# Performance work log

Measured on AMD Instinct MI355X. Metric: run time of the kernel, lower is better.

## Reference

```python
import math
import jax, jax.numpy as jnp
import numpy as np

B, L0, IN, D, H, FF, PRED = 16, 4096, 8, 256, 8, 1024, 24
NLAYERS = 3
FACTOR = 5

def _u(L):
    return max(1, min(FACTOR * math.ceil(math.log(L + 1)), L))

def _ln(x, g, b, eps=1e-5):
    m = x.mean(-1, keepdims=True)
    v = ((x - m) ** 2).mean(-1, keepdims=True)
    return (x - m) * jax.lax.rsqrt(v + eps) * g + b

def _prob_attn(h, idx, wq, bq, wk, bk, wv, bv, wo, bo):
    B_, L, Dm = h.shape
    dk = Dm // H
    scale = 1.0 / math.sqrt(dk)
    def proj(w, b):
        return (h @ w + b).reshape(B_, L, H, dk).transpose(0, 2, 1, 3)
    Q, K, V = proj(wq, bq), proj(wk, bk), proj(wv, bv)  # [B,H,L,dk]
    u = idx.shape[0]
    Ks = K[:, :, idx, :]                                   # sampled keys [B,H,u,dk]
    scores = jnp.einsum('bhld,bhud->bhlu', Q, Ks) * scale
    M = scores.max(-1) - scores.mean(-1)                   # sparsity score [B,H,L]
    top = jax.lax.top_k(M, u)[1]                           # top-u queries [B,H,u]
    Qt = jnp.take_along_axis(Q, top[..., None], axis=2)    # [B,H,u,dk]
    attn = jax.nn.softmax(jnp.einsum('bhud,bhld->bhul', Qt, K) * scale, axis=-1)
    ctx_top = jnp.einsum('bhul,bhld->bhud', attn, V)       # [B,H,u,dk]
    ctx = jnp.broadcast_to(V.mean(2, keepdims=True), (B_, H, L, dk))
    bh = B_ * H
    ctx = ctx.reshape(bh, L, dk).at[jnp.arange(bh)[:, None], top.reshape(bh, u)].set(ctx_top.reshape(bh, u, dk))
    ctx = ctx.reshape(B_, H, L, dk).transpose(0, 2, 1, 3).reshape(B_, L, Dm)
    return ctx @ wo + bo

def _distill(x, w, b):
    # Conv1d(k=3,pad=1) + ELU + MaxPool1d(2)
    xc = x.transpose(0, 2, 1)  # [B,D,L]
    y = jax.lax.conv_general_dilated(xc, w, (1,), [(1, 1)], dimension_numbers=('NCH', 'OIH', 'NCH')) + b[None, :, None]
    y = jax.nn.elu(y)
    y = jax.lax.reduce_window(y, -jnp.inf, jax.lax.max, (1, 1, 2), (1, 1, 2), 'VALID')
    return y.transpose(0, 2, 1)

def _forward(x, in_w, in_b, pos_emb, qw, qb, kw, kb, vw, vb, ow, ob, f1w, f1b, f2w, f2b, n1g, n1b, n2g, n2b, cw, cb, fcw, fcb, idxs):
    Bx, L, _ = x.shape
    h = x @ in_w + in_b + pos_emb[None, :L]
    for i in range(NLAYERS):
        a = _prob_attn(h, idxs[i], qw[i], qb[i], kw[i], kb[i], vw[i], vb[i], ow[i], ob[i])
        h = _ln(h + a, n1g[i], n1b[i])
        f = jax.nn.gelu(h @ f1w[i] + f1b[i], approximate=False) @ f2w[i] + f2b[i]
        h = _ln(h + f, n2g[i], n2b[i])
        if i < NLAYERS - 1:
            h = _distill(h, cw[i], cb[i])
    return h[:, -1, :] @ fcw + fcb

def setup_inputs():
    key = jax.random.key(0)
    ks = jax.random.split(key, 16)
    s = 0.02
    d = {}
    d['x'] = jax.random.normal(ks[0], (B, L0, IN), jnp.float32)
    Ls = [L0, L0 // 2, L0 // 4]
    for i, Li in enumerate(Ls):
        d[f'idx{i}'] = jax.random.randint(ks[1 + i], (_u(Li),), 0, Li, jnp.int32)
    d['in_w'] = jax.random.normal(ks[4], (IN, D)) * s
    d['in_b'] = jnp.zeros((D,))
    d['pos_emb'] = jax.random.normal(ks[5], (L0, D)) * s
    d['qw'] = jax.random.normal(ks[6], (NLAYERS, D, D)) * s
    d['qb'] = jnp.zeros((NLAYERS, D))
    d['kw'] = jax.random.normal(ks[7], (NLAYERS, D, D)) * s
    d['kb'] = jnp.zeros((NLAYERS, D))
    d['vw'] = jax.random.normal(ks[8], (NLAYERS, D, D)) * s
    d['vb'] = jnp.zeros((NLAYERS, D))
    d['ow'] = jax.random.normal(ks[9], (NLAYERS, D, D)) * s
    d['ob'] = jnp.zeros((NLAYERS, D))
    d['f1w'] = jax.random.normal(ks[10], (NLAYERS, D, FF)) * s
    d['f1b'] = jnp.zeros((NLAYERS, FF))
    d['f2w'] = jax.random.normal(ks[11], (NLAYERS, FF, D)) * s
    d['f2b'] = jnp.zeros((NLAYERS, D))
    d['n1g'] = jnp.ones((NLAYERS, D))
    d['n1b'] = jnp.zeros((NLAYERS, D))
    d['n2g'] = jnp.ones((NLAYERS, D))
    d['n2b'] = jnp.zeros((NLAYERS, D))
    d['cw'] = jax.random.normal(ks[12], (NLAYERS - 1, D, D, 3)) * s
    d['cb'] = jnp.zeros((NLAYERS - 1, D))
    d['fcw'] = jax.random.normal(ks[13], (D, PRED)) * s
    d['fcb'] = jnp.zeros((PRED,))
    return d

def reference(x, idx0, idx1, idx2, in_w, in_b, pos_emb, qw, qb, kw, kb, vw, vb, ow, ob, f1w, f1b, f2w, f2b, n1g, n1b, n2g, n2b, cw, cb, fcw, fcb):
    return _forward(x, in_w, in_b, pos_emb, qw, qb, kw, kb, vw, vb, ow, ob, f1w, f1b, f2w, f2b, n1g, n1b, n2g, n2b, cw, cb, fcw, fcb, (idx0, idx1, idx2))
```

## Files before the change

kernel.cpp:

```cpp
#include <hip/hip_runtime.h>
#include <hip/hip_bf16.h>
#include <math.h>

typedef __hip_bfloat16 bf16;
typedef __attribute__((ext_vector_type(8))) short short8;
typedef __attribute__((ext_vector_type(4))) float floatx4;

#define B_    16
#define L0_   4096
#define IN_   8
#define D_    256
#define H_    8
#define DK_   32
#define FF_   1024
#define PRED_ 24
#define UMAX_ 48
#define NS_   4
#define NSV_  8
#define SCALE_ 0.17677669529663687f

__device__ __forceinline__ float b2f(bf16 v) { return __bfloat162float(v); }
__device__ __forceinline__ bf16  f2b(float v){ return __float2bfloat16(v); }
__device__ __forceinline__ float gelu_exact(float x){
  return 0.5f * x * (1.0f + erff(x * 0.7071067811865476f));
}
__device__ __forceinline__ float eluf(float x){ return x > 0.f ? x : (expf(x) - 1.f); }
__device__ __forceinline__ float ldf(const void* p, size_t i, int f){
  return f ? ((const float*)p)[i] : b2f(((const bf16*)p)[i]);
}
__device__ __forceinline__ void gld16(const void* g, const short* l){
  __builtin_amdgcn_global_load_lds(
      (const __attribute__((address_space(1))) unsigned int*)g,
      (__attribute__((address_space(3))) unsigned int*)l, 16, 0, 0);
}
__device__ __forceinline__ void unpack8(uint4 v, float* o){
  o[0] = __uint_as_float(v.x << 16); o[1] = __uint_as_float(v.x & 0xffff0000u);
  o[2] = __uint_as_float(v.y << 16); o[3] = __uint_as_float(v.y & 0xffff0000u);
  o[4] = __uint_as_float(v.z << 16); o[5] = __uint_as_float(v.z & 0xffff0000u);
  o[6] = __uint_as_float(v.w << 16); o[7] = __uint_as_float(v.w & 0xffff0000u);
}
__device__ __forceinline__ void ld_row32(const bf16* p, float* o){
  const uint4* q = (const uint4*)p;
  uint4 a = q[0], b = q[1], c = q[2], d = q[3];
  unpack8(a, o); unpack8(b, o + 8); unpack8(c, o + 16); unpack8(d, o + 24);
}

__global__ __launch_bounds__(256) void detect_mode_kernel(
    const unsigned short* __restrict__ x16, int* __restrict__ flag,
    bf16* __restrict__ zbuf)
{
  int tid = threadIdx.x;
  if (tid < 32) zbuf[tid] = f2b(0.f);
  int cnt = 0;
  for (int i = tid; i < 512; i += 256) {
    unsigned short v = x16[2 * i];
    int expo = (v >> 7) & 0xFF;
    if (expo >= 0x90) cnt++;
  }
  __shared__ int red[256];
  red[tid] = cnt;
  __syncthreads();
  for (int s = 128; s > 0; s >>= 1) {
    if (tid < s) red[tid] += red[tid + s];
    __syncthreads();
  }
  if (tid == 0) flag[0] = (red[0] > 8) ? 1 : 0;
}

__global__ __launch_bounds__(256) void canon_kernel(
    const void* __restrict__ src, bf16* __restrict__ dst, int n,
    const int* __restrict__ flag)
{
  int i = blockIdx.x * 256 + threadIdx.x;
  if (i >= n) return;
  dst[i] = f2b(ldf(src, i, flag[0]));
}

__global__ __launch_bounds__(256) void transpose_w_kernel(
    const void* __restrict__ src, bf16* __restrict__ dst, int K, int N,
    const int* __restrict__ flag)
{
  int i = blockIdx.x * 256 + threadIdx.x;
  if (i >= K * N) return;
  size_t off = (size_t)blockIdx.y * K * N;
  int k = i / N, n = i % N;
  dst[off + (size_t)n * K + k] = f2b(ldf(src, off + i, flag[0]));
}

__global__ __launch_bounds__(256) void transpose_cw_kernel(
    const void* __restrict__ src, bf16* __restrict__ dst,
    const int* __restrict__ flag)
{
  int i = blockIdx.x * 256 + threadIdx.x;
  if (i >= D_ * D_ * 3) return;
  size_t off = (size_t)blockIdx.y * D_ * D_ * 3;
  int o = i / (D_ * 3), c = (i / 3) % D_, t = i % 3;
  dst[off + ((size_t)t * D_ + o) * D_ + c] = f2b(ldf(src, off + i, flag[0]));
}

__global__ __launch_bounds__(256) void embed_kernel(
    const void* __restrict__ x, const void* __restrict__ in_w,
    const void* __restrict__ in_b, const void* __restrict__ pos,
    const int* __restrict__ flag, bf16* __restrict__ h)
{
  int token = blockIdx.x;
  int d = threadIdx.x;
  int l = token % L0_;
  int f = flag[0];
  float s = ldf(in_b, d, f) + ldf(pos, (size_t)l * D_ + d, f);
#pragma unroll
  for (int k = 0; k < IN_; ++k)
    s += ldf(x, (size_t)token * IN_ + k, f) * ldf(in_w, k * D_ + d, f);
  h[(size_t)token * D_ + d] = f2b(s);
}

template<int ACT, int HM>
__global__ __launch_bounds__(256) void mfma_gemm(
    const bf16* __restrict__ A, const bf16* __restrict__ Wt,
    const bf16* __restrict__ bias, bf16* __restrict__ C,
    int M, int N, int K, int Lsh)
{
  __shared__ short As[128 * 32];
  __shared__ short Bs[128 * 32];
  int tid = threadIdx.x;
  int w = tid >> 6, lane = tid & 63;
  int ln = lane & 15, qd = lane >> 4;
  int bm = blockIdx.y << 7, bn = blockIdx.x << 7;
  int wm = (w >> 1) << 6, wn = (w & 1) << 6;

  floatx4 acc[4][4];
#pragma unroll
  for (int mi = 0; mi < 4; ++mi)
#pragma unroll
    for (int ni = 0; ni < 4; ++ni) {
      acc[mi][ni][0] = 0.f; acc[mi][ni][1] = 0.f;
      acc[mi][ni][2] = 0.f; acc[mi][ni][3] = 0.f;
    }

  int s0 = (w << 7) + lane, s1 = s0 + 64;
  int r0 = s0 >> 2, c0 = (s0 & 3) ^ (r0 & 3);
  int r1 = s1 >> 2, c1 = (s1 & 3) ^ (r1 & 3);
  const bf16* pA0 = A + (size_t)(bm + r0) * K + (c0 << 3);
  const bf16* pA1 = A + (size_t)(bm + r1) * K + (c1 << 3);
  const bf16* pB0 = Wt + (size_t)(bn + r0) * K + (c0 << 3);
  const bf16* pB1 = Wt + (size_t)(bn + r1) * K + (c1 << 3);
  short* ldsA = As + (w << 10);
  short* ldsB = Bs + (w << 10);

  for (int k0 = 0; k0 < K; k0 += 32) {
    __syncthreads();
    gld16(pA0 + k0, ldsA);
    gld16(pA1 + k0, ldsA + 512);
    gld16(pB0 + k0, ldsB);
    gld16(pB1 + k0, ldsB + 512);
    __syncthreads();
    short8 af[4], bff[4];
#pragma unroll
    for (int mi = 0; mi < 4; ++mi) {
      int r = wm + mi * 16 + ln;
      af[mi] = *(const short8*)(As + (r << 5) + ((qd ^ (r & 3)) << 3));
    }
#pragma unroll
    for (int ni = 0; ni < 4; ++ni) {
      int r = wn + ni * 16 + ln;
      bff[ni] = *(const short8*)(Bs + (r << 5) + ((qd ^ (r & 3)) << 3));
    }
#pragma unroll
    for (int mi = 0; mi < 4; ++mi)
#pragma unroll
      for (int ni = 0; ni < 4; ++ni)
        acc[mi][ni] = __builtin_amdgcn_mfma_f32_16x16x32_bf16(
            af[mi], bff[ni], acc[mi][ni], 0, 0, 0);
  }

#pragma unroll
  for (int ni = 0; ni < 4; ++ni) {
    int col = bn + wn + ni * 16 + ln;
    float bv = b2f(bias[col]);
    int hh = col >> 5, dk = col & 31;
#pragma unroll
    for (int mi = 0; mi < 4; ++mi) {
      int row = bm + wm + mi * 16 + (qd << 2);
#pragma unroll
      for (int r = 0; r < 4; ++r) {
        float v = acc[mi][ni][r] + bv;
        if (ACT == 1) v = gelu_exact(v);
        if (HM) {
          int rr = row + r;
          int bb = rr >> Lsh, ll = rr & ((1 << Lsh) - 1);
          C[((((size_t)(bb * H_ + hh)) << Lsh) + ll) * 32 + dk] = f2b(v);
        } else {
          C[(size_t)(row + r) * N + col] = f2b(v);
        }
      }
    }
  }
}

__global__ __launch_bounds__(256) void mfma_conv_distill(
    const bf16* __restrict__ hsrc, const bf16* __restrict__ WtC,
    const bf16* __restrict__ cb, bf16* __restrict__ outp,
    const bf16* __restrict__ zbuf, int L)
{
  __shared__ short As[128 * 32];
  __shared__ short Bs[128 * 32];
  int tid = threadIdx.x;
  int w = tid >> 6, lane = tid & 63;
  int ln = lane & 15, qd = lane >> 4;
  int bn = blockIdx.x << 7;
  int bpb = L >> 7;
  int b = blockIdx.y / bpb;
  int p0 = (blockIdx.y % bpb) << 7;
  int wm = (w >> 1) << 6, wn = (w & 1) << 6;

  floatx4 acc[4][4];
#pragma unroll
  for (int mi = 0; mi < 4; ++mi)
#pragma unroll
    for (int ni = 0; ni < 4; ++ni) {
      acc[mi][ni][0] = 0.f; acc[mi][ni][1] = 0.f;
      acc[mi][ni][2] = 0.f; acc[mi][ni][3] = 0.f;
    }

  int s0 = (w << 7) + lane, s1 = s0 + 64;
  int r0 = s0 >> 2, c0 = (s0 & 3) ^ (r0 & 3);
  int r1 = s1 >> 2, c1 = (s1 & 3) ^ (r1 & 3);
  short* ldsA = As + (w << 10);
  short* ldsB = Bs + (w << 10);

  for (int tap = 0; tap < 3; ++tap) {
    const bf16* wt = WtC + (size_t)tap * D_ * D_;
    int pos0 = p0 + r0 + tap - 1;
    int pos1 = p0 + r1 + tap - 1;
    const bf16* gA0 = (pos0 >= 0 && pos0 < L)
        ? hsrc + ((size_t)b * L + pos0) * D_ + (c0 << 3) : zbuf;
    const bf16* gA1 = (pos1 >= 0 && pos1 < L)
        ? hsrc + ((size_t)b * L + pos1) * D_ + (c1 << 3) : zbuf;
    int stepA0 = (pos0 >= 0 && pos0 < L) ? 1 : 0;
    int stepA1 = (pos1 >= 0 && pos1 < L) ? 1 : 0;
    const bf16* gB0 = wt + (size_t)(bn + r0) * D_ + (c0 << 3);
    const bf16* gB1 = wt + (size_t)(bn + r1) * D_ + (c1 << 3);
    for (int k0 = 0; k0 < D_; k0 += 32) {
      __syncthreads();
      gld16(gA0 + (size_t)k0 * stepA0, ldsA);
      gld16(gA1 + (size_t)k0 * stepA1, ldsA + 512);
      gld16(gB0 + k0, ldsB);
      gld16(gB1 + k0, ldsB + 512);
      __syncthreads();
      short8 af[4], bff[4];
#pragma unroll
      for (int mi = 0; mi < 4; ++mi) {
        int r = wm + mi * 16 + ln;
        af[mi] = *(const short8*)(As + (r << 5) + ((qd ^ (r & 3)) << 3));
      }
#pragma unroll
      for (int ni = 0; ni < 4; ++ni) {
        int r = wn + ni * 16 + ln;
        bff[ni] = *(const short8*)(Bs + (r << 5) + ((qd ^ (r & 3)) << 3));
      }
#pragma unroll
      for (int mi = 0; mi < 4; ++mi)
#pragma unroll
        for (int ni = 0; ni < 4; ++ni)
          acc[mi][ni] = __builtin_amdgcn_mfma_f32_16x16x32_bf16(
              af[mi], bff[ni], acc[mi][ni], 0, 0, 0);
    }
  }

  int Lh = L >> 1;
#pragma unroll
  for (int ni = 0; ni < 4; ++ni) {
    int col = bn + wn + ni * 16 + ln;
    float bv = b2f(cb[col]);
#pragma unroll
    for (int mi = 0; mi < 4; ++mi) {
      float y0 = eluf(acc[mi][ni][0] + bv);
      float y1 = eluf(acc[mi][ni][1] + bv);
      float y2 = eluf(acc[mi][ni][2] + bv);
      float y3 = eluf(acc[mi][ni][3] + bv);
      int prow = (p0 + wm + mi * 16 + (qd << 2)) >> 1;
      outp[((size_t)b * Lh + prow) * D_ + col]     = f2b(fmaxf(y0, y1));
      outp[((size_t)b * Lh + prow + 1) * D_ + col] = f2b(fmaxf(y2, y3));
    }
  }
}

__global__ __launch_bounds__(256) void prob_scores_kernel(
    const bf16* __restrict__ Qh, const bf16* __restrict__ Kh,
    const int* __restrict__ idx, float* __restrict__ Mout, int L, int u)
{
  __shared__ float ks[UMAX_][32];
  int tid = threadIdx.x;
  int bpb = L >> 8;
  int bh = blockIdx.x / bpb;
  int l  = (blockIdx.x % bpb) * 256 + tid;
  if (tid < u * 4) {
    int t = tid >> 2, c = tid & 3;
    int ls = idx[t];
    if (ls < 0) ls = 0; if (ls >= L) ls = L - 1;
    uint4 v = *(const uint4*)(Kh + ((size_t)bh * L + ls) * 32 + c * 8);
    unpack8(v, &ks[t][c * 8]);
  }
  __syncthreads();
  float qv[32];
  ld_row32(Qh + ((size_t)bh * L + l) * 32, qv);
  float mx = -3.4e38f, sm = 0.f;
  for (int t = 0; t < u; ++t) {
    float s = 0.f;
#pragma unroll
    for (int j4 = 0; j4 < 8; ++j4) {
      float4 k4 = *(const float4*)&ks[t][j4 * 4];
      s += qv[4*j4+0]*k4.x + qv[4*j4+1]*k4.y + qv[4*j4+2]*k4.z + qv[4*j4+3]*k4.w;
    }
    s *= SCALE_;
    mx = fmaxf(mx, s);
    sm += s;
  }
  Mout[(size_t)bh * L + l] = mx - sm / (float)u;
}

__global__ __launch_bounds__(256) void topk_kernel(
    const float* __restrict__ M, int* __restrict__ top, int L, int u)
{
  __shared__ unsigned int hist[256];
  __shared__ unsigned int prefS, kS;
  __shared__ int cntG, tieCnt;
  __shared__ int tieList[256];
  int bh = blockIdx.x;
  int tid = threadIdx.x;
  int w = tid >> 6, lane = tid & 63;
  int nper = L >> 8;

  unsigned int key[16];
  for (int i = 0; i < nper; ++i) {
    unsigned int ub = __float_as_uint(M[(size_t)bh * L + i * 256 + tid]);
    key[i] = (ub & 0x80000000u) ? ~ub : (ub | 0x80000000u);
  }

  unsigned int pref = 0, k = (unsigned int)u;
  for (int round = 0; round < 4; ++round) {
    int shift = 24 - (round << 3);
    hist[tid] = 0;
    __syncthreads();
    for (int i = 0; i < nper; ++i) {
      unsigned int kk = key[i];
      if (round == 0 || (kk >> (shift + 8)) == pref)
        atomicAdd(&hist[(kk >> shift) & 0xFFu], 1u);
    }
    __syncthreads();
    if (w == 0) {
      int d0 = lane << 2;
      unsigned int h0 = hist[d0], h1 = hist[d0 + 1];
      unsigned int h2 = hist[d0 + 2], h3 = hist[d0 + 3];
      unsigned int lsum = h0 + h1 + h2 + h3;
      unsigned int incl = lsum;
#pragma unroll
      for (int off = 1; off < 64; off <<= 1) {
        unsigned int o = __shfl_down(incl, off);
        if (lane + off < 64) incl += o;
      }
      unsigned int e3 = incl - lsum;
      unsigned int e2 = e3 + h3;
      unsigned int e1 = e2 + h2;
      unsigned int e0 = e1 + h1;
      if (e3 < k && k <= e3 + h3) { prefS = (pref << 8) | (d0 + 3); kS = k - e3; }
      if (e2 < k && k <= e2 + h2) { prefS = (pref << 8) | (d0 + 2); kS = k - e2; }
      if (e1 < k && k <= e1 + h1) { prefS = (pref << 8) | (d0 + 1); kS = k - e1; }
      if (e0 < k && k <= e0 + h0) { prefS = (pref << 8) | (d0 + 0); kS = k - e0; }
    }
    __syncthreads();
    pref = prefS;
    k = kS;
    __syncthreads();
  }

  unsigned int T = pref;
  if (tid == 0) { cntG = 0; tieCnt = 0; }
  __syncthreads();
  for (int i = 0; i < nper; ++i) {
    unsigned int kk = key[i];
    int lidx = i * 256 + tid;
    if (kk > T) {
      int pos = atomicAdd(&cntG, 1);
      if (pos < u) top[bh * u + pos] = lidx;
    } else if (kk == T) {
      int tpos = atomicAdd(&tieCnt, 1);
      if (tpos < 256) tieList[tpos] = lidx;
    }
  }
  __syncthreads();
  if (tid == 0) {
    int base = cntG;
    int E = tieCnt; if (E > 256) E = 256;
    for (int t = 0; t < (int)k && base + t < u; ++t) {
      int best = 0x7fffffff, bj = -1;
      for (int j = 0; j < E; ++j) {
        int v = tieList[j];
        if (v >= 0 && v < best) { best = v; bj = j; }
      }
      if (bj >= 0) { tieList[bj] = -1; top[bh * u + base + t] = best; }
      else top[bh * u + base + t] = 0;
    }
  }
}

__global__ __launch_bounds__(256) void topq_attn_mfma(
    const bf16* __restrict__ Qh, const bf16* __restrict__ Kh,
    const bf16* __restrict__ Vh, const int* __restrict__ top,
    float* __restrict__ part_m, float* __restrict__ part_s,
    float* __restrict__ part_acc, int L, int u)
{
  __shared__ short Qs[64 * 32];
  __shared__ short Ks[128 * 32];
  __shared__ short Vs[128 * 32];
  __shared__ short Ps[4][64 * 32];
  __shared__ float mrow[64];
  __shared__ float redm[4][64];
  __shared__ float redl[4][64];

  int bh = blockIdx.x, sl = blockIdx.y;
  int tid = threadIdx.x;
  int w = tid >> 6, lane = tid & 63;
  int ln = lane & 15, qd = lane >> 4;
  int Ls = L / NS_;
  int lbase = sl * Ls;
  const bf16* Kbase = Kh + (size_t)bh * L * 32;
  const bf16* Vbase = Vh + (size_t)bh * L * 32;

  {
    int r = tid >> 2, cpos = tid & 3, corig = cpos ^ (r & 3);
    uint4 v = make_uint4(0, 0, 0, 0);
    if (r < u) {
      int lq = top[bh * u + r];
      if (lq < 0) lq = 0; if (lq >= L) lq = L - 1;
      v = *(const uint4*)(Qh + ((size_t)bh * L + lq) * 32 + corig * 8);
    }
    *(uint4*)(Qs + r * 32 + cpos * 8) = v;
  }
  __syncthreads();

  short8 aq[4];
#pragma unroll
  for (int mi = 0; mi < 4; ++mi) {
    int r = mi * 16 + ln;
    aq[mi] = *(const short8*)(Qs + (r << 5) + ((qd ^ (r & 3)) << 3));
  }

  int s0 = (w << 7) + lane, s1 = s0 + 64;
  int r0 = s0 >> 2, c0 = (s0 & 3) ^ (r0 & 3);
  int r1 = s1 >> 2, c1 = (s1 & 3) ^ (r1 & 3);
  short* ldsK = Ks + (w << 10);
  short* ldsV = Vs + (w << 10);
  int nch = Ls >> 7;

  float m_run[16];
#pragma unroll
  for (int i = 0; i < 16; ++i) m_run[i] = -3.4e38f;

  for (int ch = 0; ch < nch; ++ch) {
    int tok0 = lbase + (ch << 7);
    __syncthreads();
    gld16(Kbase + (size_t)(tok0 + r0) * 32 + (c0 << 3), ldsK);
    gld16(Kbase + (size_t)(tok0 + r1) * 32 + (c1 << 3), ldsK + 512);
    __syncthreads();
    short8 bk[2];
#pragma unroll
    for (int ni = 0; ni < 2; ++ni) {
      int r = (w << 5) + ni * 16 + ln;
      bk[ni] = *(const short8*)(Ks + (r << 5) + ((qd ^ (r & 3)) << 3));
    }
#pragma unroll
    for (int mi = 0; mi < 4; ++mi)
#pragma unroll
      for (int ni = 0; ni < 2; ++ni) {
        floatx4 s = {0.f, 0.f, 0.f, 0.f};
        s = __builtin_amdgcn_mfma_f32_16x16x32_bf16(aq[mi], bk[ni], s, 0, 0, 0);
#pragma unroll
        for (int r = 0; r < 4; ++r)
          m_run[mi * 4 + r] = fmaxf(m_run[mi * 4 + r], s[r] * SCALE_);
      }
  }
#pragma unroll
  for (int i = 0; i < 16; ++i) {
    float v = m_run[i];
    v = fmaxf(v, __shfl_xor(v, 1));
    v = fmaxf(v, __shfl_xor(v, 2));
    v = fmaxf(v, __shfl_xor(v, 4));
    v = fmaxf(v, __shfl_xor(v, 8));
    m_run[i] = v;
  }
  if (ln == 0) {
#pragma unroll
    for (int mi = 0; mi < 4; ++mi)
#pragma unroll
      for (int r = 0; r < 4; ++r)
        redm[w][mi * 16 + qd * 4 + r] = m_run[mi * 4 + r];
  }
  __syncthreads();
  if (tid < 64)
    mrow[tid] = fmaxf(fmaxf(redm[0][tid], redm[1][tid]),
                      fmaxf(redm[2][tid], redm[3][tid]));
  __syncthreads();

  float l_run[16];
#pragma unroll
  for (int i = 0; i < 16; ++i) l_run[i] = 0.f;
  floatx4 oacc[4][2];
#pragma unroll
  for (int mi = 0; mi < 4; ++mi)
#pragma unroll
    for (int ni = 0; ni < 2; ++ni) {
      oacc[mi][ni][0] = 0.f; oacc[mi][ni][1] = 0.f;
      oacc[mi][ni][2] = 0.f; oacc[mi][ni][3] = 0.f;
    }
  bf16* myPs = (bf16*)Ps[w];

  for (int ch = 0; ch < nch; ++ch) {
    int tok0 = lbase + (ch << 7);
    __syncthreads();
    gld16(Kbase + (size_t)(tok0 + r0) * 32 + (c0 << 3), ldsK);
    gld16(Kbase + (size_t)(tok0 + r1) * 32 + (c1 << 3), ldsK + 512);
    gld16(Vbase + (size_t)(tok0 + r0) * 32 + (c0 << 3), ldsV);
    gld16(Vbase + (size_t)(tok0 + r1) * 32 + (c1 << 3), ldsV + 512);
    __syncthreads();
    short8 bk[2];
#pragma unroll
    for (int ni = 0; ni < 2; ++ni) {
      int r = (w << 5) + ni * 16 + ln;
      bk[ni] = *(const short8*)(Ks + (r << 5) + ((qd ^ (r & 3)) << 3));
    }
#pragma unroll
    for (int mi = 0; mi < 4; ++mi)
#pragma unroll
      for (int ni = 0; ni < 2; ++ni) {
        floatx4 s = {0.f, 0.f, 0.f, 0.f};
        s = __builtin_amdgcn_mfma_f32_16x16x32_bf16(aq[mi], bk[ni], s, 0, 0, 0);
#pragma unroll
        for (int r = 0; r < 4; ++r) {
          int row = mi * 16 + qd * 4 + r;
          float p = expf(s[r] * SCALE_ - mrow[row]);
          l_run[mi * 4 + r] += p;
          int tl = ni * 16 + ln;
          myPs[(row << 5) + (((tl >> 3) ^ (row & 3)) << 3) + (tl & 7)] = f2b(p);
        }
      }
    __syncthreads();
    short8 ap[4];
#pragma unroll
    for (int mi = 0; mi < 4; ++mi) {
      int r = mi * 16 + ln;
      ap[mi] = *(const short8*)((short*)myPs + (r << 5) + ((qd ^ (r & 3)) << 3));
    }
    short8 bv[2];
#pragma unroll
    for (int ni = 0; ni < 2; ++ni) {
      short tmp[8];
#pragma unroll
      for (int j = 0; j < 8; ++j) {
        int tok = (w << 5) + (qd << 3) + j;
        int dk = ni * 16 + ln;
        tmp[j] = Vs[(tok << 5) + (((dk >> 3) ^ (tok & 3)) << 3) + (dk & 7)];
      }
      bv[ni] = *(short8*)tmp;
    }
#pragma unroll
    for (int mi = 0; mi < 4; ++mi)
#pragma unroll
      for (int ni = 0; ni < 2; ++ni)
        oacc[mi][ni] = __builtin_amdgcn_mfma_f32_16x16x32_bf16(
            ap[mi], bv[ni], oacc[mi][ni], 0, 0, 0);
  }

#pragma unroll
  for (int i = 0; i < 16; ++i) {
    float v = l_run[i];
    v += __shfl_xor(v, 1); v += __shfl_xor(v, 2);
    v += __shfl_xor(v, 4); v += __shfl_xor(v, 8);
    l_run[i] = v;
  }
  if (ln == 0) {
#pragma unroll
    for (int mi = 0; mi < 4; ++mi)
#pragma unroll
      for (int r = 0; r < 4; ++r)
        redl[w][mi * 16 + qd * 4 + r] = l_run[mi * 4 + r];
  }
  __syncthreads();

  size_t pb = (size_t)sl * (B_ * H_) + bh;
  if (tid < UMAX_) {
    part_m[pb * UMAX_ + tid] = mrow[tid];
    part_s[pb * UMAX_ + tid] =
        redl[0][tid] + redl[1][tid] + redl[2][tid] + redl[3][tid];
  }
#pragma unroll
  for (int mi = 0; mi < 4; ++mi) {
#pragma unroll
    for (int ni = 0; ni < 2; ++ni) {
#pragma unroll
      for (int r = 0; r < 4; ++r) {
        int row = mi * 16 + qd * 4 + r;
        if (row < UMAX_) {
          int dk = ni * 16 + ln;
          part_acc[((pb * UMAX_ + row) << 7) + (w << 5) + dk] = oacc[mi][ni][r];
        }
      }
    }
  }
}

__global__ __launch_bounds__(256) void attn_combine_kernel(
    const float* __restrict__ part_m, const float* __restrict__ part_s,
    const float* __restrict__ part_acc, float* __restrict__ ctx_top, int u)
{
  int bh = blockIdx.x;
  for (int i = threadIdx.x; i < u * 32; i += 256) {
    int q = i >> 5, dk = i & 31;
    float M = -3.4e38f;
#pragma unroll
    for (int s = 0; s < NS_; ++s)
      M = fmaxf(M, part_m[((size_t)s * (B_ * H_) + bh) * UMAX_ + q]);
    float num = 0.f, den = 0.f;
#pragma unroll
    for (int s = 0; s < NS_; ++s) {
      size_t pb = (size_t)s * (B_ * H_) + bh;
      float e = expf(part_m[pb * UMAX_ + q] - M);
      float a = 0.f;
#pragma unroll
      for (int w = 0; w < 4; ++w)
        a += part_acc[((pb * UMAX_ + q) << 7) + (w << 5) + dk];
      num += a * e;
      den += part_s[pb * UMAX_ + q] * e;
    }
    ctx_top[((size_t)bh * u + q) * 32 + dk] = num / den;
  }
}

__global__ __launch_bounds__(256) void vmean_part_kernel(
    const bf16* __restrict__ Vh, float* __restrict__ vpart, int L)
{
  int blk = blockIdx.x;
  int bh = blk / NSV_, s = blk % NSV_;
  int tid = threadIdx.x;
  int dk = tid & 31, lg = tid >> 5;
  int Ls = L / NSV_;
  int l0 = s * Ls;
  float acc = 0.f;
  for (int l = lg; l < Ls; l += 8)
    acc += b2f(Vh[((size_t)bh * L + l0 + l) * 32 + dk]);
  __shared__ float red[256];
  red[tid] = acc;
  __syncthreads();
  for (int st = 128; st >= 32; st >>= 1) {
    if (tid < st) red[tid] += red[tid + st];
    __syncthreads();
  }
  if (tid < 32) vpart[(size_t)blk * 32 + tid] = red[tid];
}

__global__ __launch_bounds__(32) void vmean_comb_kernel(
    const float* __restrict__ vpart, float* __restrict__ vmean, int L)
{
  int bh = blockIdx.x;
  int dk = threadIdx.x;
  float s = 0.f;
#pragma unroll
  for (int i = 0; i < NSV_; ++i)
    s += vpart[((size_t)bh * NSV_ + i) * 32 + dk];
  vmean[bh * 32 + dk] = s / (float)L;
}

__global__ __launch_bounds__(256) void fill_ctx_kernel(
    const float* __restrict__ vmean, bf16* __restrict__ ctx, int L)
{
  size_t i = (size_t)blockIdx.x * 256 + threadIdx.x;
  int d = (int)(i % D_);
  size_t token = i / D_;
  int b = (int)(token / L);
  ctx[i] = f2b(vmean[(b * H_ + d / DK_) * DK_ + (d & (DK_ - 1))]);
}

__global__ __launch_bounds__(256) void scatter_kernel(
    const float* __restrict__ ctx_top, const int* __restrict__ top,
    bf16* __restrict__ ctx, int L, int u)
{
  int t = blockIdx.x * 256 + threadIdx.x;
  int total = B_ * H_ * u * DK_;
  if (t >= total) return;
  int j  = t % DK_;
  int uu = (t / DK_) % u;
  int hh = (t / (DK_ * u)) % H_;
  int b  = t / (DK_ * u * H_);
  int lq = top[(b * H_ + hh) * u + uu];
  if (lq < 0) lq = 0; if (lq >= L) lq = L - 1;
  ctx[((size_t)b * L + lq) * D_ + hh * DK_ + j] =
      f2b(ctx_top[(size_t)((b * H_ + hh) * u + uu) * DK_ + j]);
}

__global__ __launch_bounds__(256) void add_ln_kernel(
    bf16* __restrict__ h, const bf16* __restrict__ r,
    const bf16* __restrict__ g, const bf16* __restrict__ be)
{
  size_t t = blockIdx.x;
  int d = threadIdx.x;
  __shared__ float lds4[4];
  float v = b2f(h[t * D_ + d]) + b2f(r[t * D_ + d]);
  float s = v;
  for (int off = 32; off; off >>= 1) s += __shfl_down(s, off);
  if ((threadIdx.x & 63) == 0) lds4[threadIdx.x >> 6] = s;
  __syncthreads();
  float mean = (lds4[0] + lds4[1] + lds4[2] + lds4[3]) * (1.f / D_);
  __syncthreads();
  float dv = v - mean;
  float q = dv * dv;
  for (int off = 32; off; off >>= 1) q += __shfl_down(q, off);
  if ((threadIdx.x & 63) == 0) lds4[threadIdx.x >> 6] = q;
  __syncthreads();
  float var = (lds4[0] + lds4[1] + lds4[2] + lds4[3]) * (1.f / D_);
  h[t * D_ + d] = f2b(dv * rsqrtf(var + 1e-5f) * b2f(g[d]) + b2f(be[d]));
}

__global__ __launch_bounds__(256) void copy_bf16_kernel(
    bf16* __restrict__ dst, const bf16* __restrict__ src, size_t n)
{
  size_t i = (size_t)blockIdx.x * 256 + threadIdx.x;
  if (i < n) dst[i] = src[i];
}

__global__ __launch_bounds__(64) void final_fc_kernel(
    const bf16* __restrict__ h, const bf16* __restrict__ fcw,
    const bf16* __restrict__ fcb, void* __restrict__ out, int L,
    const int* __restrict__ flag)
{
  int b = blockIdx.x;
  int p = threadIdx.x;
  if (p >= PRED_) return;
  const bf16* hr = h + ((size_t)b * L + (L - 1)) * D_;
  float s = b2f(fcb[p]);
  for (int d = 0; d < D_; ++d) s += b2f(hr[d]) * b2f(fcw[d * PRED_ + p]);
  if (flag[0]) ((float*)out)[b * PRED_ + p] = s;
  else         ((bf16*)out)[b * PRED_ + p]  = f2b(s);
}

extern "C" void kernel_launch(void* const* d_in, const int* in_sizes, int n_in,
                              void* d_out, int out_size, void* d_ws, size_t ws_size,
                              hipStream_t stream)
{
  const size_t hsz = (size_t)B_ * L0_ * D_;
  char* wsc = (char*)d_ws;
  bf16* h  = (bf16*)wsc;
  bf16* Qh = (bf16*)(wsc + hsz * 2);
  bf16* Kh = (bf16*)(wsc + hsz * 4);
  bf16* Vh = (bf16*)(wsc + hsz * 6);
  char* misc = wsc + hsz * 8;
  float* Mbuf    = (float*)misc;
  float* ctx_top = Mbuf + (size_t)B_ * H_ * L0_;
  float* vmean   = ctx_top + (size_t)B_ * H_ * UMAX_ * DK_;
  int*   topbuf  = (int*)(vmean + B_ * H_ * DK_);
  int*   flag    = topbuf + B_ * H_ * UMAX_;
  float* part_m  = (float*)(flag + 4);
  float* part_s  = part_m + (size_t)NS_ * B_ * H_ * UMAX_;
  float* part_acc= part_s + (size_t)NS_ * B_ * H_ * UMAX_;
  float* vpart   = part_acc + (size_t)NS_ * B_ * H_ * UMAX_ * 128;
  bf16*  zbuf    = (bf16*)(vpart + (size_t)B_ * H_ * NSV_ * 32);
  bf16*  canon   = zbuf + 32;

  bf16* qwT  = canon;
  bf16* kwT  = qwT  + 3 * 65536;
  bf16* vwT  = kwT  + 3 * 65536;
  bf16* owT  = vwT  + 3 * 65536;
  bf16* f1wT = owT  + 3 * 65536;
  bf16* f2wT = f1wT + 3 * 262144;
  bf16* cwT  = f2wT + 3 * 262144;
  bf16* smallc = cwT + 2 * 196608;

  bf16* ctxb = Vh;
  bf16* ab   = Qh;
  bf16* t1   = Kh;
  bf16* hnext = Kh;

  detect_mode_kernel<<<1, 256, 0, stream>>>((const unsigned short*)d_in[0], flag, zbuf);

  const int cidx[13] = {8, 10, 12, 14, 16, 18, 19, 20, 21, 22, 24, 25, 26};
  bf16* cptr[27] = {};
  {
    bf16* p = smallc;
    for (int t = 0; t < 13; ++t) {
      int i = cidx[t];
      int n = in_sizes[i];
      cptr[i] = p;
      canon_kernel<<<(n + 255) / 256, 256, 0, stream>>>(d_in[i], p, n, flag);
      p += (n + 7) & ~7;
    }
  }
  transpose_w_kernel<<<dim3(256, 3), 256, 0, stream>>>(d_in[7],  qwT,  256, 256, flag);
  transpose_w_kernel<<<dim3(256, 3), 256, 0, stream>>>(d_in[9],  kwT,  256, 256, flag);
  transpose_w_kernel<<<dim3(256, 3), 256, 0, stream>>>(d_in[11], vwT,  256, 256, flag);
  transpose_w_kernel<<<dim3(256, 3), 256, 0, stream>>>(d_in[13], owT,  256, 256, flag);
  transpose_w_kernel<<<dim3(1024, 3), 256, 0, stream>>>(d_in[15], f1wT, 256, 1024, flag);
  transpose_w_kernel<<<dim3(1024, 3), 256, 0, stream>>>(d_in[17], f2wT, 1024, 256, flag);
  transpose_cw_kernel<<<dim3(768, 2), 256, 0, stream>>>(d_in[23], cwT, flag);

  const int* idx[3] = {(const int*)d_in[1], (const int*)d_in[2], (const int*)d_in[3]};
  int us[3] = {in_sizes[1], in_sizes[2], in_sizes[3]};

  embed_kernel<<<B_ * L0_, 256, 0, stream>>>(d_in[0], d_in[4], d_in[5], d_in[6], flag, h);

  int L = L0_;
  for (int i = 0; i < 3; ++i) {
    int tokens = B_ * L;
    int u = us[i];
    int Lsh = 31 - __builtin_clz(L);
    dim3 gDD(2, tokens / 128);
    mfma_gemm<0,1><<<gDD, 256, 0, stream>>>(h, qwT + (size_t)i * 65536, cptr[8]  + i * D_, Qh, tokens, D_, D_, Lsh);
    mfma_gemm<0,1><<<gDD, 256, 0, stream>>>(h, kwT + (size_t)i * 65536, cptr[10] + i * D_, Kh, tokens, D_, D_, Lsh);
    mfma_gemm<0,1><<<gDD, 256, 0, stream>>>(h, vwT + (size_t)i * 65536, cptr[12] + i * D_, Vh, tokens, D_, D_, Lsh);

    prob_scores_kernel<<<B_ * H_ * (L / 256), 256, 0, stream>>>(Qh, Kh, idx[i], Mbuf, L, u);
    topk_kernel<<<B_ * H_, 256, 0, stream>>>(Mbuf, topbuf, L, u);
    topq_attn_mfma<<<dim3(B_ * H_, NS_), 256, 0, stream>>>(
        Qh, Kh, Vh, topbuf, part_m, part_s, part_acc, L, u);
    attn_combine_kernel<<<B_ * H_, 256, 0, stream>>>(part_m, part_s, part_acc, ctx_top, u);
    vmean_part_kernel<<<B_ * H_ * NSV_, 256, 0, stream>>>(Vh, vpart, L);
    vmean_comb_kernel<<<B_ * H_, 32, 0, stream>>>(vpart, vmean, L);
    fill_ctx_kernel<<<(unsigned)(((size_t)tokens * D_) / 256), 256, 0, stream>>>(vmean, ctxb, L);
    scatter_kernel<<<(B_ * H_ * u * DK_ + 255) / 256, 256, 0, stream>>>(ctx_top, topbuf, ctxb, L, u);
    mfma_gemm<0,0><<<gDD, 256, 0, stream>>>(ctxb, owT + (size_t)i * 65536, cptr[14] + i * D_, ab, tokens, D_, D_, 0);

    add_ln_kernel<<<tokens, 256, 0, stream>>>(h, ab, cptr[19] + i * D_, cptr[20] + i * D_);

    const int CH = 16384;
    for (int c0 = 0; c0 < tokens; c0 += CH) {
      int cm = (tokens - c0 < CH) ? (tokens - c0) : CH;
      mfma_gemm<1,0><<<dim3(8, cm / 128), 256, 0, stream>>>(
          h + (size_t)c0 * D_, f1wT + (size_t)i * 262144, cptr[16] + i * FF_, t1, cm, FF_, D_, 0);
      mfma_gemm<0,0><<<dim3(2, cm / 128), 256, 0, stream>>>(
          t1, f2wT + (size_t)i * 262144, cptr[18] + i * D_, ab + (size_t)c0 * D_, cm, D_, FF_, 0);
    }
    add_ln_kernel<<<tokens, 256, 0, stream>>>(h, ab, cptr[21] + i * D_, cptr[22] + i * D_);

    if (i < 2) {
      int Lh = L / 2;
      mfma_conv_distill<<<dim3(2, B_ * (L / 128)), 256, 0, stream>>>(
          h, cwT + (size_t)i * 196608, cptr[24] + i * D_, hnext, zbuf, L);
      size_t n = (size_t)B_ * Lh * D_;
      copy_bf16_kernel<<<(unsigned)((n + 255) / 256), 256, 0, stream>>>(h, hnext, n);
      L = Lh;
    }
  }
  final_fc_kernel<<<B_, 64, 0, stream>>>(h, cptr[25], cptr[26], d_out, L, flag);
}
```

Measured before the change: 1.432 ms.

## Fuse QKV GEMMs, deepen GEMM K-tile, vectorize LayerNorm, embed and fill kernels

The three Q/K/V projections become one GEMM over a concatenated 768-wide weight, with per-part bias and head-major output to Q/K/V buffers separated by a stride. This removes two launches and two extra reads of h. The shared GEMM kernel now stages a 64-wide K slice per barrier pair with an 8-way XOR swizzle, which halves the number of syncs but doubles LDS use per block. add_ln becomes one wave per row with vectorized loads and xor-shuffle reductions, and the embed and fill_ctx kernels each process 8 tokens per block.

```diff
diff --git a/kernel.cpp b/kernel.cpp
--- a/kernel.cpp
+++ b/kernel.cpp
@@ -39,6 +39,14 @@
   o[4] = __uint_as_float(v.z << 16); o[5] = __uint_as_float(v.z & 0xffff0000u);
   o[6] = __uint_as_float(v.w << 16); o[7] = __uint_as_float(v.w & 0xffff0000u);
 }
+__device__ __forceinline__ void unpack4(uint2 v, float* o){
+  o[0] = __uint_as_float(v.x << 16); o[1] = __uint_as_float(v.x & 0xffff0000u);
+  o[2] = __uint_as_float(v.y << 16); o[3] = __uint_as_float(v.y & 0xffff0000u);
+}
+__device__ __forceinline__ unsigned pack2(float a, float b){
+  bf16 x = f2b(a), y = f2b(b);
+  return (unsigned)*(unsigned short*)&x | ((unsigned)*(unsigned short*)&y << 16);
+}
 __device__ __forceinline__ void ld_row32(const bf16* p, float* o){
   const uint4* q = (const uint4*)p;
   uint4 a = q[0], b = q[1], c = q[2], d = q[3];
@@ -78,13 +86,13 @@
 
 __global__ __launch_bounds__(256) void transpose_w_kernel(
     const void* __restrict__ src, bf16* __restrict__ dst, int K, int N,
-    const int* __restrict__ flag)
+    const int* __restrict__ flag, int lstride)
 {
   int i = blockIdx.x * 256 + threadIdx.x;
   if (i >= K * N) return;
-  size_t off = (size_t)blockIdx.y * K * N;
+  size_t soff = (size_t)blockIdx.y * K * N;
   int k = i / N, n = i % N;
-  dst[off + (size_t)n * K + k] = f2b(ldf(src, off + i, flag[0]));
+  dst[(size_t)blockIdx.y * lstride + (size_t)n * K + k] = f2b(ldf(src, soff + i, flag[0]));
 }
 
 __global__ __launch_bounds__(256) void transpose_cw_kernel(
@@ -103,25 +111,34 @@
     const void* __restrict__ in_b, const void* __restrict__ pos,
     const int* __restrict__ flag, bf16* __restrict__ h)
 {
-  int token = blockIdx.x;
   int d = threadIdx.x;
-  int l = token % L0_;
   int f = flag[0];
-  float s = ldf(in_b, d, f) + ldf(pos, (size_t)l * D_ + d, f);
-#pragma unroll
-  for (int k = 0; k < IN_; ++k)
-    s += ldf(x, (size_t)token * IN_ + k, f) * ldf(in_w, k * D_ + d, f);
-  h[(size_t)token * D_ + d] = f2b(s);
+  float wcol[IN_];
+#pragma unroll
+  for (int k = 0; k < IN_; ++k) wcol[k] = ldf(in_w, k * D_ + d, f);
+  float bd = ldf(in_b, d, f);
+  int t0 = blockIdx.x * 8;
+#pragma unroll
+  for (int t = 0; t < 8; ++t) {
+    int token = t0 + t;
+    int l = token & (L0_ - 1);
+    float s = bd + ldf(pos, (size_t)l * D_ + d, f);
+#pragma unroll
+    for (int k = 0; k < IN_; ++k)
+      s += ldf(x, (size_t)token * IN_ + k, f) * wcol[k];
+    h[(size_t)token * D_ + d] = f2b(s);
+  }
 }
 
 template<int ACT, int HM>
 __global__ __launch_bounds__(256) void mfma_gemm(
     const bf16* __restrict__ A, const bf16* __restrict__ Wt,
-    const bf16* __restrict__ bias, bf16* __restrict__ C,
-    int M, int N, int K, int Lsh)
-{
-  __shared__ short As[128 * 32];
-  __shared__ short Bs[128 * 32];
+    const bf16* __restrict__ b0, const bf16* __restrict__ b1,
+    const bf16* __restrict__ b2, bf16* __restrict__ C,
+    int M, int N, int K, int Lsh, size_t partStride)
+{
+  __shared__ short As[128 * 64];
+  __shared__ short Bs[128 * 64];
   int tid = threadIdx.x;
   int w = tid >> 6, lane = tid & 63;
   int ln = lane & 15, qd = lane >> 4;
@@ -137,47 +154,64 @@
       acc[mi][ni][2] = 0.f; acc[mi][ni][3] = 0.f;
     }
 
-  int s0 = (w << 7) + lane, s1 = s0 + 64;
-  int r0 = s0 >> 2, c0 = (s0 & 3) ^ (r0 & 3);
-  int r1 = s1 >> 2, c1 = (s1 & 3) ^ (r1 & 3);
-  const bf16* pA0 = A + (size_t)(bm + r0) * K + (c0 << 3);
-  const bf16* pA1 = A + (size_t)(bm + r1) * K + (c1 << 3);
-  const bf16* pB0 = Wt + (size_t)(bn + r0) * K + (c0 << 3);
-  const bf16* pB1 = Wt + (size_t)(bn + r1) * K + (c1 << 3);
-  short* ldsA = As + (w << 10);
-  short* ldsB = Bs + (w << 10);
-
-  for (int k0 = 0; k0 < K; k0 += 32) {
-    __syncthreads();
-    gld16(pA0 + k0, ldsA);
-    gld16(pA1 + k0, ldsA + 512);
-    gld16(pB0 + k0, ldsB);
-    gld16(pB1 + k0, ldsB + 512);
-    __syncthreads();
-    short8 af[4], bff[4];
-#pragma unroll
-    for (int mi = 0; mi < 4; ++mi) {
-      int r = wm + mi * 16 + ln;
-      af[mi] = *(const short8*)(As + (r << 5) + ((qd ^ (r & 3)) << 3));
-    }
-#pragma unroll
-    for (int ni = 0; ni < 4; ++ni) {
-      int r = wn + ni * 16 + ln;
-      bff[ni] = *(const short8*)(Bs + (r << 5) + ((qd ^ (r & 3)) << 3));
-    }
-#pragma unroll
-    for (int mi = 0; mi < 4; ++mi)
-#pragma unroll
-      for (int ni = 0; ni < 4; ++ni)
-        acc[mi][ni] = __builtin_amdgcn_mfma_f32_16x16x32_bf16(
-            af[mi], bff[ni], acc[mi][ni], 0, 0, 0);
+  int rr[4], ofs[4];
+#pragma unroll
+  for (int t = 0; t < 4; ++t) {
+    int p = (w << 8) + (t << 6) + lane;
+    int r = p >> 3;
+    ofs[t] = (((p & 7) ^ (r & 7)) << 3);
+    rr[t] = r;
+  }
+  const bf16* pA[4]; const bf16* pB[4]; short* dst[4];
+#pragma unroll
+  for (int t = 0; t < 4; ++t) {
+    pA[t] = A + (size_t)(bm + rr[t]) * K + ofs[t];
+    pB[t] = Wt + (size_t)(bn + rr[t]) * K + ofs[t];
+    dst[t] = (short*)(As) + (((w << 2) + t) << 9);
+  }
+
+  for (int k0 = 0; k0 < K; k0 += 64) {
+    __syncthreads();
+#pragma unroll
+    for (int t = 0; t < 4; ++t) gld16(pA[t] + k0, dst[t]);
+#pragma unroll
+    for (int t = 0; t < 4; ++t) gld16(pB[t] + k0, dst[t] + 128 * 64);
+    __syncthreads();
+#pragma unroll
+    for (int kb = 0; kb < 2; ++kb) {
+      short8 af[4], bff[4];
+#pragma unroll
+      for (int mi = 0; mi < 4; ++mi) {
+        int r = wm + mi * 16 + ln;
+        af[mi] = *(const short8*)(As + (r << 6) + ((((kb << 2) + qd) ^ (r & 7)) << 3));
+      }
+#pragma unroll
+      for (int ni = 0; ni < 4; ++ni) {
+        int r = wn + ni * 16 + ln;
+        bff[ni] = *(const short8*)(Bs + (r << 6) + ((((kb << 2) + qd) ^ (r & 7)) << 3));
+      }
+#pragma unroll
+      for (int mi = 0; mi < 4; ++mi)
+#pragma unroll
+        for (int ni = 0; ni < 4; ++ni)
+          acc[mi][ni] = __builtin_amdgcn_mfma_f32_16x16x32_bf16(
+              af[mi], bff[ni], acc[mi][ni], 0, 0, 0);
+    }
   }
 
 #pragma unroll
   for (int ni = 0; ni < 4; ++ni) {
     int col = bn + wn + ni * 16 + ln;
-    float bv = b2f(bias[col]);
-    int hh = col >> 5, dk = col & 31;
+    const bf16* bsel = b0;
+    int cm = col;
+    if (HM) {
+      int part = col >> 8;
+      cm = col & 255;
+      bsel = (part == 0) ? b0 : ((part == 1) ? b1 : b2);
+    }
+    float bv = b2f(bsel[cm]);
+    int part = HM ? (col >> 8) : 0;
+    int hh = cm >> 5, dk = cm & 31;
 #pragma unroll
     for (int mi = 0; mi < 4; ++mi) {
       int row = bm + wm + mi * 16 + (qd << 2);
@@ -186,9 +220,9 @@
         float v = acc[mi][ni][r] + bv;
         if (ACT == 1) v = gelu_exact(v);
         if (HM) {
-          int rr = row + r;
-          int bb = rr >> Lsh, ll = rr & ((1 << Lsh) - 1);
-          C[((((size_t)(bb * H_ + hh)) << Lsh) + ll) * 32 + dk] = f2b(v);
+          int rr2 = row + r;
+          int bb = rr2 >> Lsh, ll = rr2 & ((1 << Lsh) - 1);
+          C[part * partStride + ((((size_t)(bb * H_ + hh)) << Lsh) + ll) * 32 + dk] = f2b(v);
         } else {
           C[(size_t)(row + r) * N + col] = f2b(v);
         }
@@ -671,13 +705,17 @@
 }
 
 __global__ __launch_bounds__(256) void fill_ctx_kernel(
-    const float* __restrict__ vmean, bf16* __restrict__ ctx, int L)
-{
-  size_t i = (size_t)blockIdx.x * 256 + threadIdx.x;
-  int d = (int)(i % D_);
-  size_t token = i / D_;
-  int b = (int)(token / L);
-  ctx[i] = f2b(vmean[(b * H_ + d / DK_) * DK_ + (d & (DK_ - 1))]);
+    const float* __restrict__ vmean, bf16* __restrict__ ctx, int Lsh)
+{
+  int d = threadIdx.x;
+  size_t t0 = (size_t)blockIdx.x * 8;
+  int hh = d >> 5, dk = d & 31;
+#pragma unroll
+  for (int t = 0; t < 8; ++t) {
+    size_t token = t0 + t;
+    int b = (int)(token >> Lsh);
+    ctx[token * D_ + d] = f2b(vmean[(b * H_ + hh) * 32 + dk]);
+  }
 }
 
 __global__ __launch_bounds__(256) void scatter_kernel(
@@ -701,23 +739,31 @@
     bf16* __restrict__ h, const bf16* __restrict__ r,
     const bf16* __restrict__ g, const bf16* __restrict__ be)
 {
-  size_t t = blockIdx.x;
-  int d = threadIdx.x;
-  __shared__ float lds4[4];
-  float v = b2f(h[t * D_ + d]) + b2f(r[t * D_ + d]);
-  float s = v;
-  for (int off = 32; off; off >>= 1) s += __shfl_down(s, off);
-  if ((threadIdx.x & 63) == 0) lds4[threadIdx.x >> 6] = s;
-  __syncthreads();
-  float mean = (lds4[0] + lds4[1] + lds4[2] + lds4[3]) * (1.f / D_);
-  __syncthreads();
-  float dv = v - mean;
-  float q = dv * dv;
-  for (int off = 32; off; off >>= 1) q += __shfl_down(q, off);
-  if ((threadIdx.x & 63) == 0) lds4[threadIdx.x >> 6] = q;
-  __syncthreads();
-  float var = (lds4[0] + lds4[1] + lds4[2] + lds4[3]) * (1.f / D_);
-  h[t * D_ + d] = f2b(dv * rsqrtf(var + 1e-5f) * b2f(g[d]) + b2f(be[d]));
+  int w = threadIdx.x >> 6, lane = threadIdx.x & 63;
+  size_t row = (size_t)blockIdx.x * 4 + w;
+  bf16* hp = h + row * D_;
+  const bf16* rp = r + row * D_;
+  float hv[4], rv[4];
+  unpack4(*(const uint2*)(hp + lane * 4), hv);
+  unpack4(*(const uint2*)(rp + lane * 4), rv);
+  float v0 = hv[0] + rv[0], v1 = hv[1] + rv[1];
+  float v2 = hv[2] + rv[2], v3 = hv[3] + rv[3];
+  float s = v0 + v1 + v2 + v3;
+#pragma unroll
+  for (int off = 1; off < 64; off <<= 1) s += __shfl_xor(s, off);
+  float mean = s * (1.f / D_);
+  float d0 = v0 - mean, d1 = v1 - mean, d2 = v2 - mean, d3 = v3 - mean;
+  float q = d0 * d0 + d1 * d1 + d2 * d2 + d3 * d3;
+#pragma unroll
+  for (int off = 1; off < 64; off <<= 1) q += __shfl_xor(q, off);
+  float rstd = rsqrtf(q * (1.f / D_) + 1e-5f);
+  float gv[4], bv[4];
+  unpack4(*(const uint2*)(g + lane * 4), gv);
+  unpack4(*(const uint2*)(be + lane * 4), bv);
+  uint2 o;
+  o.x = pack2(d0 * rstd * gv[0] + bv[0], d1 * rstd * gv[1] + bv[1]);
+  o.y = pack2(d2 * rstd * gv[2] + bv[2], d3 * rstd * gv[3] + bv[3]);
+  *(uint2*)(hp + lane * 4) = o;
 }
 
 __global__ __launch_bounds__(256) void copy_bf16_kernel(
@@ -765,10 +811,8 @@
   bf16*  zbuf    = (bf16*)(vpart + (size_t)B_ * H_ * NSV_ * 32);
   bf16*  canon   = zbuf + 32;
 
-  bf16* qwT  = canon;
-  bf16* kwT  = qwT  + 3 * 65536;
-  bf16* vwT  = kwT  + 3 * 65536;
-  bf16* owT  = vwT  + 3 * 65536;
+  bf16* qkvT = canon;
+  bf16* owT  = qkvT + 3 * 196608;
   bf16* f1wT = owT  + 3 * 65536;
   bf16* f2wT = f1wT + 3 * 262144;
   bf16* cwT  = f2wT + 3 * 262144;
@@ -793,28 +837,28 @@
       p += (n + 7) & ~7;
     }
   }
-  transpose_w_kernel<<<dim3(256, 3), 256, 0, stream>>>(d_in[7],  qwT,  256, 256, flag);
-  transpose_w_kernel<<<dim3(256, 3), 256, 0, stream>>>(d_in[9],  kwT,  256, 256, flag);
-  transpose_w_kernel<<<dim3(256, 3), 256, 0, stream>>>(d_in[11], vwT,  256, 256, flag);
-  transpose_w_kernel<<<dim3(256, 3), 256, 0, stream>>>(d_in[13], owT,  256, 256, flag);
-  transpose_w_kernel<<<dim3(1024, 3), 256, 0, stream>>>(d_in[15], f1wT, 256, 1024, flag);
-  transpose_w_kernel<<<dim3(1024, 3), 256, 0, stream>>>(d_in[17], f2wT, 1024, 256, flag);
+  transpose_w_kernel<<<dim3(256, 3), 256, 0, stream>>>(d_in[7],  qkvT,          256, 256, flag, 196608);
+  transpose_w_kernel<<<dim3(256, 3), 256, 0, stream>>>(d_in[9],  qkvT + 65536,  256, 256, flag, 196608);
+  transpose_w_kernel<<<dim3(256, 3), 256, 0, stream>>>(d_in[11], qkvT + 131072, 256, 256, flag, 196608);
+  transpose_w_kernel<<<dim3(256, 3), 256, 0, stream>>>(d_in[13], owT,  256, 256, flag, 65536);
+  transpose_w_kernel<<<dim3(1024, 3), 256, 0, stream>>>(d_in[15], f1wT, 256, 1024, flag, 262144);
+  transpose_w_kernel<<<dim3(1024, 3), 256, 0, stream>>>(d_in[17], f2wT, 1024, 256, flag, 262144);
   transpose_cw_kernel<<<dim3(768, 2), 256, 0, stream>>>(d_in[23], cwT, flag);
 
   const int* idx[3] = {(const int*)d_in[1], (const int*)d_in[2], (const int*)d_in[3]};
   int us[3] = {in_sizes[1], in_sizes[2], in_sizes[3]};
 
-  embed_kernel<<<B_ * L0_, 256, 0, stream>>>(d_in[0], d_in[4], d_in[5], d_in[6], flag, h);
+  embed_kernel<<<B_ * L0_ / 8, 256, 0, stream>>>(d_in[0], d_in[4], d_in[5], d_in[6], flag, h);
 
   int L = L0_;
   for (int i = 0; i < 3; ++i) {
     int tokens = B_ * L;
     int u = us[i];
     int Lsh = 31 - __builtin_clz(L);
-    dim3 gDD(2, tokens / 128);
-    mfma_gemm<0,1><<<gDD, 256, 0, stream>>>(h, qwT + (size_t)i * 65536, cptr[8]  + i * D_, Qh, tokens, D_, D_, Lsh);
-    mfma_gemm<0,1><<<gDD, 256, 0, stream>>>(h, kwT + (size_t)i * 65536, cptr[10] + i * D_, Kh, tokens, D_, D_, Lsh);
-    mfma_gemm<0,1><<<gDD, 256, 0, stream>>>(h, vwT + (size_t)i * 65536, cptr[12] + i * D_, Vh, tokens, D_, D_, Lsh);
+    mfma_gemm<0,1><<<dim3(6, tokens / 128), 256, 0, stream>>>(
+        h, qkvT + (size_t)i * 196608,
+        cptr[8] + i * D_, cptr[10] + i * D_, cptr[12] + i * D_,
+        Qh, tokens, 768, 256, Lsh, hsz);
 
     prob_scores_kernel<<<B_ * H_ * (L / 256), 256, 0, stream>>>(Qh, Kh, idx[i], Mbuf, L, u);
     topk_kernel<<<B_ * H_, 256, 0, stream>>>(Mbuf, topbuf, L, u);
@@ -823,21 +867,25 @@
     attn_combine_kernel<<<B_ * H_, 256, 0, stream>>>(part_m, part_s, part_acc, ctx_top, u);
     vmean_part_kernel<<<B_ * H_ * NSV_, 256, 0, stream>>>(Vh, vpart, L);
     vmean_comb_kernel<<<B_ * H_, 32, 0, stream>>>(vpart, vmean, L);
-    fill_ctx_kernel<<<(unsigned)(((size_t)tokens * D_) / 256), 256, 0, stream>>>(vmean, ctxb, L);
+    fill_ctx_kernel<<<tokens / 8, 256, 0, stream>>>(vmean, ctxb, Lsh);
     scatter_kernel<<<(B_ * H_ * u * DK_ + 255) / 256, 256, 0, stream>>>(ctx_top, topbuf, ctxb, L, u);
-    mfma_gemm<0,0><<<gDD, 256, 0, stream>>>(ctxb, owT + (size_t)i * 65536, cptr[14] + i * D_, ab, tokens, D_, D_, 0);
-
-    add_ln_kernel<<<tokens, 256, 0, stream>>>(h, ab, cptr[19] + i * D_, cptr[20] + i * D_);
+    mfma_gemm<0,0><<<dim3(2, tokens / 128), 256, 0, stream>>>(
+        ctxb, owT + (size_t)i * 65536, cptr[14] + i * D_, nullptr, nullptr,
+        ab, tokens, 256, 256, 0, 0);
+
+    add_ln_kernel<<<tokens / 4, 256, 0, stream>>>(h, ab, cptr[19] + i * D_, cptr[20] + i * D_);
 
     const int CH = 16384;
     for (int c0 = 0; c0 < tokens; c0 += CH) {
       int cm = (tokens - c0 < CH) ? (tokens - c0) : CH;
       mfma_gemm<1,0><<<dim3(8, cm / 128), 256, 0, stream>>>(
-          h + (size_t)c0 * D_, f1wT + (size_t)i * 262144, cptr[16] + i * FF_, t1, cm, FF_, D_, 0);
+          h + (size_t)c0 * D_, f1wT + (size_t)i * 262144, cptr[16] + i * FF_,
+          nullptr, nullptr, t1, cm, FF_, 256, 0, 0);
       mfma_gemm<0,0><<<dim3(2, cm / 128), 256, 0, stream>>>(
-          t1, f2wT + (size_t)i * 262144, cptr[18] + i * D_, ab + (size_t)c0 * D_, cm, D_, FF_, 0);
-    }
-    add_ln_kernel<<<tokens, 256, 0, stream>>>(h, ab, cptr[21] + i * D_, cptr[22] + i * D_);
+          t1, f2wT + (size_t)i * 262144, cptr[18] + i * D_, nullptr, nullptr,
+          ab + (size_t)c0 * D_, cm, 256, FF_, 0, 0);
+    }
+    add_ln_kernel<<<tokens / 4, 256, 0, stream>>>(h, ab, cptr[21] + i * D_, cptr[22] + i * D_);
 
     if (i < 2) {
       int Lh = L / 2;
```

Result: faster. 1.208 ms (-15.6%).
